# Optimization experiments

Hardware: AMD Instinct MI355X
Metric: run time of the kernel (lower is better)

## Reference

```python
import jax, jax.numpy as jnp
import numpy as np

EPS = 1e-5

def exp_map_zero(v):
    # Poincare ball exp map at origin: tanh(||v||) * v / ||v||
    norm = jnp.clip(jnp.linalg.norm(v, axis=-1, keepdims=True), EPS, None)
    return jnp.tanh(jnp.clip(norm, None, 15.0)) * v / norm

def poincare_pairwise_distance(x, c):
    # x: [N, D] points in the ball, c: [K, D] points in the ball -> [N, K]
    x2 = jnp.sum(x * x, axis=-1)                      # [N]
    c2 = jnp.sum(c * c, axis=-1)                      # [K]
    sqdiff = x2[:, None] + c2[None, :] - 2.0 * (x @ c.T)   # ||x-c||^2, [N, K]
    sqdiff = jnp.clip(sqdiff, 0.0, None)
    denom = jnp.clip((1.0 - x2)[:, None] * (1.0 - c2)[None, :], EPS, None)
    arg = jnp.clip(1.0 + 2.0 * sqdiff / denom, 1.0 + 1e-7, None)
    return jnp.arccosh(arg)

def setup_inputs() -> dict:
    key = jax.random.key(0)
    k1, k2, k3 = jax.random.split(key, 3)
    N, K, D = 200000, 128, 128
    node_repr = jax.random.normal(k1, (N, D), dtype=jnp.float32) * 0.05  # inside unit ball
    mask = jnp.ones((N, 1), dtype=jnp.float32)
    centroid_weight = jax.random.normal(k2, (K, D), dtype=jnp.float32) * 0.05
    return {"node_repr": node_repr, "mask": mask, "centroid_weight": centroid_weight}

def reference(node_repr, mask, centroid_weight):
    # euclidean embed_manifold path: map centroid params onto the ball first
    centroid_repr = exp_map_zero(centroid_weight)                  # [K, D]
    dist = poincare_pairwise_distance(node_repr, centroid_repr)    # [N, K]
    node_centroid_dist = dist[None, :, :] * mask                   # [1, N, K] (mask [N,1] broadcasts)
    graph_centroid_dist = jnp.sum(node_centroid_dist, axis=1) / jnp.sum(mask)  # [1, K]
    return (graph_centroid_dist, node_centroid_dist)
```

## Files before the change

### kernel.cpp

```cpp
#include <hip/hip_runtime.h>
#include <hip/hip_bf16.h>
#include <math.h>

#define EPSF 1e-5f

constexpr int D = 128;
constexpr int K = 128;
constexpr int ROWS_PER_BLOCK = 64;
constexpr int BPITCH = 272;

typedef __bf16 bf16x8 __attribute__((ext_vector_type(8)));
typedef float  f32x4  __attribute__((ext_vector_type(4)));

__global__ __launch_bounds__(64) void prep_kernel(const float* __restrict__ w,
                                                  __bf16* __restrict__ crb,
                                                  float* __restrict__ c2) {
    int k = blockIdx.x;
    int t = threadIdx.x;
    float a = w[k * D + t];
    float b = w[k * D + t + 64];
    float ss = a * a + b * b;
#pragma unroll
    for (int off = 1; off < 64; off <<= 1)
        ss += __shfl_xor(ss, off, 64);
    float nrm   = sqrtf(ss);
    float nclip = fmaxf(nrm, EPSF);
    float targ  = fminf(nclip, 15.0f);
    float th    = tanhf(targ);
    float s     = th / nclip;
    crb[k * D + t]      = (__bf16)(a * s);
    crb[k * D + t + 64] = (__bf16)(b * s);
    if (t == 0) {
        float cn = s * nrm;
        c2[k] = cn * cn;
    }
}

__global__ __launch_bounds__(256) void main_kernel(
        const float* __restrict__ x, const float* __restrict__ mask,
        const __bf16* __restrict__ crb, const float* __restrict__ c2g,
        float* __restrict__ out_node, float* __restrict__ partial,
        float* __restrict__ maskpart, int N) {
    __shared__ __align__(16) unsigned char sB[K * BPITCH];
    __shared__ float sX2[ROWS_PER_BLOCK];
    __shared__ float sMask[ROWS_PER_BLOCK];
    __shared__ float sC2[K];
    __shared__ float sCol[4][K];

    const int t    = threadIdx.x;
    const int wave = t >> 6;
    const int lane = t & 63;
    const int m    = lane & 15;
    const int q    = lane >> 4;
    const int nbase   = blockIdx.x * ROWS_PER_BLOCK;
    const int rowbase = nbase + wave * 16;

    const float* xrow = x + (size_t)(rowbase + m) * D + q * 8;
    float4 xr[8];
#pragma unroll
    for (int s = 0; s < 4; s++) {
        xr[2 * s]     = *(const float4*)(xrow + s * 32);
        xr[2 * s + 1] = *(const float4*)(xrow + s * 32 + 4);
    }

#pragma unroll
    for (int i = 0; i < 8; i++) {
        int f4  = t + 256 * i;
        int row = f4 >> 4;
        int c4  = f4 & 15;
        float4 v = ((const float4*)crb)[f4];
        *(float4*)(sB + row * BPITCH + c4 * 16) = v;
    }
    if (t < ROWS_PER_BLOCK) sMask[t] = mask[nbase + t];
    if (t < K) sC2[t] = c2g[t];

    float ssq = 0.f;
    bf16x8 av[4];
#pragma unroll
    for (int s = 0; s < 4; s++) {
        float4 a0 = xr[2 * s], a1 = xr[2 * s + 1];
        ssq += a0.x*a0.x + a0.y*a0.y + a0.z*a0.z + a0.w*a0.w
             + a1.x*a1.x + a1.y*a1.y + a1.z*a1.z + a1.w*a1.w;
        av[s][0] = (__bf16)a0.x; av[s][1] = (__bf16)a0.y;
        av[s][2] = (__bf16)a0.z; av[s][3] = (__bf16)a0.w;
        av[s][4] = (__bf16)a1.x; av[s][5] = (__bf16)a1.y;
        av[s][6] = (__bf16)a1.z; av[s][7] = (__bf16)a1.w;
    }
    ssq += __shfl_xor(ssq, 16, 64);
    ssq += __shfl_xor(ssq, 32, 64);
    if (lane < 16) sX2[wave * 16 + lane] = ssq;

    __syncthreads();

    f32x4 acc[8] = {};
#pragma unroll
    for (int s = 0; s < 4; s++) {
#pragma unroll
        for (int tk = 0; tk < 8; tk++) {
            bf16x8 bv = *(const bf16x8*)(sB + (tk * 16 + m) * BPITCH + q * 16 + s * 64);
            acc[tk] = __builtin_amdgcn_mfma_f32_16x16x32_bf16(av[s], bv, acc[tk], 0, 0, 0);
        }
    }

    float x2r[4], pxr[4], mvr[4];
#pragma unroll
    for (int i = 0; i < 4; i++) {
        int rl = wave * 16 + q * 4 + i;
        x2r[i] = sX2[rl];
        pxr[i] = 1.0f - x2r[i];
        mvr[i] = sMask[rl];
    }

    float dv[8][4];
    float colsum[8];
#pragma unroll
    for (int tk = 0; tk < 8; tk++) {
        int col = tk * 16 + m;
        float c2v = sC2[col];
        float pc  = 1.0f - c2v;
        colsum[tk] = 0.f;
#pragma unroll
        for (int i = 0; i < 4; i++) {
            float dot = acc[tk][i];
            float sq  = fmaxf(x2r[i] + c2v - 2.0f * dot, 0.0f);
            float den = fmaxf(pxr[i] * pc, EPSF);
            float arg = fmaf(2.0f * sq, __builtin_amdgcn_rcpf(den), 1.0f);
            arg = fmaxf(arg, 1.0f + 1e-7f);
            float dist = __logf(arg + __builtin_amdgcn_sqrtf(fmaf(arg, arg, -1.0f)));
            float val = dist * mvr[i];
            dv[tk][i] = val;
            colsum[tk] += val;
        }
    }

#pragma unroll
    for (int tk = 0; tk < 8; tk++) {
        colsum[tk] += __shfl_xor(colsum[tk], 16, 64);
        colsum[tk] += __shfl_xor(colsum[tk], 32, 64);
    }
    if (lane < 16) {
#pragma unroll
        for (int tk = 0; tk < 8; tk++)
            sCol[wave][tk * 16 + lane] = colsum[tk];
    }

    __syncthreads();

    if (t < K)
        partial[(size_t)blockIdx.x * K + t] =
            sCol[0][t] + sCol[1][t] + sCol[2][t] + sCol[3][t];
    if (t == 0) {
        float msum = 0.f;
#pragma unroll
        for (int r = 0; r < ROWS_PER_BLOCK; r++) msum += sMask[r];
        maskpart[blockIdx.x] = msum;
    }
#pragma unroll
    for (int tk = 0; tk < 8; tk++) {
        int col = tk * 16 + m;
#pragma unroll
        for (int i = 0; i < 4; i++) {
            int n = rowbase + q * 4 + i;
            __builtin_nontemporal_store(dv[tk][i], &out_node[(size_t)n * K + col]);
        }
    }
}

__global__ __launch_bounds__(256) void reduce_kernel(
        const float* __restrict__ partial, const float* __restrict__ maskpart,
        float* __restrict__ out_graph, int NB) {
    int k = blockIdx.x;
    int t = threadIdx.x;
    float s = 0.f, mm = 0.f;
    for (int b = t; b < NB; b += 256) {
        s  += partial[(size_t)b * K + k];
        mm += maskpart[b];
    }
#pragma unroll
    for (int off = 1; off < 64; off <<= 1) {
        s  += __shfl_xor(s, off, 64);
        mm += __shfl_xor(mm, off, 64);
    }
    __shared__ float rs[4], rm[4];
    int w = t >> 6;
    if ((t & 63) == 0) { rs[w] = s; rm[w] = mm; }
    __syncthreads();
    if (t == 0) {
        float st = rs[0] + rs[1] + rs[2] + rs[3];
        float mt = rm[0] + rm[1] + rm[2] + rm[3];
        out_graph[k] = st / mt;
    }
}

extern "C" void kernel_launch(void* const* d_in, const int* in_sizes, int n_in,
                              void* d_out, int out_size, void* d_ws, size_t ws_size,
                              hipStream_t stream) {
    const float* node = (const float*)d_in[0];
    const float* mask = (const float*)d_in[1];
    const float* w    = (const float*)d_in[2];
    float* out = (float*)d_out;

    int N  = in_sizes[0] / D;
    int NB = N / ROWS_PER_BLOCK;

    __bf16* crb     = (__bf16*)d_ws;
    float* c2       = (float*)(crb + K * D);
    float* partial  = c2 + K;
    float* maskpart = partial + (size_t)NB * K;

    float* out_graph = out;
    float* out_node  = out + K;

    prep_kernel<<<K, 64, 0, stream>>>(w, crb, c2);
    main_kernel<<<NB, 256, 0, stream>>>(node, mask, crb, c2, out_node,
                                        partial, maskpart, N);
    reduce_kernel<<<K, 256, 0, stream>>>(partial, maskpart, out_graph, NB);
}
```

Before: 196.8 us.

## Make main kernel persistent with software-prefetched tiles and register-resident row stats

Replaces the one-tile-per-block grid with a persistent grid of up to 1024 blocks. Each block stages the centroid matrix in LDS once, then loops over 64-row tiles, prefetching the next tile's x and mask into registers while the current tile's MFMA and epilogue run. Row norms and mask values now move through wave shuffles instead of LDS, and outputs are stored inside the epilogue. The aim is to amortize B staging, cut the per-block partial traffic and reduction size, and overlap loads with compute. The cost is more register pressure and less latency hiding from block-level parallelism.

```diff
diff --git a/kernel.cpp b/kernel.cpp
--- a/kernel.cpp
+++ b/kernel.cpp
@@ -6,8 +6,9 @@
 
 constexpr int D = 128;
 constexpr int K = 128;
-constexpr int ROWS_PER_BLOCK = 64;
+constexpr int TILE_ROWS = 64;
 constexpr int BPITCH = 272;
+constexpr int NBG = 1024;
 
 typedef __bf16 bf16x8 __attribute__((ext_vector_type(8)));
 typedef float  f32x4  __attribute__((ext_vector_type(4)));
@@ -36,32 +37,22 @@
     }
 }
 
-__global__ __launch_bounds__(256) void main_kernel(
+__global__ __launch_bounds__(256, 4) void main_kernel(
         const float* __restrict__ x, const float* __restrict__ mask,
         const __bf16* __restrict__ crb, const float* __restrict__ c2g,
         float* __restrict__ out_node, float* __restrict__ partial,
-        float* __restrict__ maskpart, int N) {
+        float* __restrict__ maskpart, int ntiles) {
     __shared__ __align__(16) unsigned char sB[K * BPITCH];
-    __shared__ float sX2[ROWS_PER_BLOCK];
-    __shared__ float sMask[ROWS_PER_BLOCK];
-    __shared__ float sC2[K];
     __shared__ float sCol[4][K];
+    __shared__ float sM[4];
 
     const int t    = threadIdx.x;
     const int wave = t >> 6;
     const int lane = t & 63;
     const int m    = lane & 15;
     const int q    = lane >> 4;
-    const int nbase   = blockIdx.x * ROWS_PER_BLOCK;
-    const int rowbase = nbase + wave * 16;
-
-    const float* xrow = x + (size_t)(rowbase + m) * D + q * 8;
-    float4 xr[8];
-#pragma unroll
-    for (int s = 0; s < 4; s++) {
-        xr[2 * s]     = *(const float4*)(xrow + s * 32);
-        xr[2 * s + 1] = *(const float4*)(xrow + s * 32 + 4);
-    }
+    const int bid  = blockIdx.x;
+    const int stride = gridDim.x;
 
 #pragma unroll
     for (int i = 0; i < 8; i++) {
@@ -71,66 +62,98 @@
         float4 v = ((const float4*)crb)[f4];
         *(float4*)(sB + row * BPITCH + c4 * 16) = v;
     }
-    if (t < ROWS_PER_BLOCK) sMask[t] = mask[nbase + t];
-    if (t < K) sC2[t] = c2g[t];
-
-    float ssq = 0.f;
+
+    float c2v[8];
+#pragma unroll
+    for (int tk = 0; tk < 8; tk++) c2v[tk] = c2g[tk * 16 + m];
+
+    float colsum[8] = {0.f, 0.f, 0.f, 0.f, 0.f, 0.f, 0.f, 0.f};
+    float msumacc = 0.f;
+
+    float4 xr[8];
+    float  mk;
     bf16x8 av[4];
-#pragma unroll
-    for (int s = 0; s < 4; s++) {
-        float4 a0 = xr[2 * s], a1 = xr[2 * s + 1];
-        ssq += a0.x*a0.x + a0.y*a0.y + a0.z*a0.z + a0.w*a0.w
-             + a1.x*a1.x + a1.y*a1.y + a1.z*a1.z + a1.w*a1.w;
-        av[s][0] = (__bf16)a0.x; av[s][1] = (__bf16)a0.y;
-        av[s][2] = (__bf16)a0.z; av[s][3] = (__bf16)a0.w;
-        av[s][4] = (__bf16)a1.x; av[s][5] = (__bf16)a1.y;
-        av[s][6] = (__bf16)a1.z; av[s][7] = (__bf16)a1.w;
-    }
-    ssq += __shfl_xor(ssq, 16, 64);
-    ssq += __shfl_xor(ssq, 32, 64);
-    if (lane < 16) sX2[wave * 16 + lane] = ssq;
+    float  x2r[4], pxr[4], mvr[4];
+
+    auto issue_loads = [&](int tl) {
+        const float* xrow = x + (size_t)(tl * TILE_ROWS + wave * 16 + m) * D + q * 8;
+#pragma unroll
+        for (int s = 0; s < 4; s++) {
+            xr[2 * s]     = *(const float4*)(xrow + s * 32);
+            xr[2 * s + 1] = *(const float4*)(xrow + s * 32 + 4);
+        }
+        mk = mask[tl * TILE_ROWS + wave * 16 + m];
+    };
+
+    auto finish_tile = [&]() {
+        float ssq = 0.f;
+#pragma unroll
+        for (int s = 0; s < 4; s++) {
+            float4 a0 = xr[2 * s], a1 = xr[2 * s + 1];
+            ssq += a0.x*a0.x + a0.y*a0.y + a0.z*a0.z + a0.w*a0.w
+                 + a1.x*a1.x + a1.y*a1.y + a1.z*a1.z + a1.w*a1.w;
+            av[s][0] = (__bf16)a0.x; av[s][1] = (__bf16)a0.y;
+            av[s][2] = (__bf16)a0.z; av[s][3] = (__bf16)a0.w;
+            av[s][4] = (__bf16)a1.x; av[s][5] = (__bf16)a1.y;
+            av[s][6] = (__bf16)a1.z; av[s][7] = (__bf16)a1.w;
+        }
+        ssq += __shfl_xor(ssq, 16, 64);
+        ssq += __shfl_xor(ssq, 32, 64);
+        float mred = mk;
+        mred += __shfl_xor(mred, 1, 64);
+        mred += __shfl_xor(mred, 2, 64);
+        mred += __shfl_xor(mred, 4, 64);
+        mred += __shfl_xor(mred, 8, 64);
+        msumacc += mred;
+#pragma unroll
+        for (int i = 0; i < 4; i++) {
+            x2r[i] = __shfl(ssq, q * 4 + i, 64);
+            pxr[i] = 1.0f - x2r[i];
+            mvr[i] = __shfl(mk, q * 4 + i, 64);
+        }
+    };
 
     __syncthreads();
 
-    f32x4 acc[8] = {};
-#pragma unroll
-    for (int s = 0; s < 4; s++) {
+    issue_loads(bid);
+    finish_tile();
+
+    for (int tile = bid; tile < ntiles; tile += stride) {
+        f32x4 acc[8] = {};
+#pragma unroll
+        for (int s = 0; s < 4; s++) {
+#pragma unroll
+            for (int tk = 0; tk < 8; tk++) {
+                bf16x8 bv = *(const bf16x8*)(sB + (tk * 16 + m) * BPITCH + q * 16 + s * 64);
+                acc[tk] = __builtin_amdgcn_mfma_f32_16x16x32_bf16(av[s], bv, acc[tk], 0, 0, 0);
+            }
+        }
+
+        int next = tile + stride;
+        bool more = next < ntiles;
+        if (more) issue_loads(next);
+
+        const int rowq = tile * TILE_ROWS + wave * 16 + q * 4;
+        float* obase = out_node + (size_t)rowq * K + m;
 #pragma unroll
         for (int tk = 0; tk < 8; tk++) {
-            bf16x8 bv = *(const bf16x8*)(sB + (tk * 16 + m) * BPITCH + q * 16 + s * 64);
-            acc[tk] = __builtin_amdgcn_mfma_f32_16x16x32_bf16(av[s], bv, acc[tk], 0, 0, 0);
-        }
-    }
-
-    float x2r[4], pxr[4], mvr[4];
-#pragma unroll
-    for (int i = 0; i < 4; i++) {
-        int rl = wave * 16 + q * 4 + i;
-        x2r[i] = sX2[rl];
-        pxr[i] = 1.0f - x2r[i];
-        mvr[i] = sMask[rl];
-    }
-
-    float dv[8][4];
-    float colsum[8];
-#pragma unroll
-    for (int tk = 0; tk < 8; tk++) {
-        int col = tk * 16 + m;
-        float c2v = sC2[col];
-        float pc  = 1.0f - c2v;
-        colsum[tk] = 0.f;
-#pragma unroll
-        for (int i = 0; i < 4; i++) {
-            float dot = acc[tk][i];
-            float sq  = fmaxf(x2r[i] + c2v - 2.0f * dot, 0.0f);
-            float den = fmaxf(pxr[i] * pc, EPSF);
-            float arg = fmaf(2.0f * sq, __builtin_amdgcn_rcpf(den), 1.0f);
-            arg = fmaxf(arg, 1.0f + 1e-7f);
-            float dist = __logf(arg + __builtin_amdgcn_sqrtf(fmaf(arg, arg, -1.0f)));
-            float val = dist * mvr[i];
-            dv[tk][i] = val;
-            colsum[tk] += val;
-        }
+            float c2c = c2v[tk];
+            float pc  = 1.0f - c2c;
+#pragma unroll
+            for (int i = 0; i < 4; i++) {
+                float dot = acc[tk][i];
+                float sq  = fmaxf(x2r[i] + c2c - 2.0f * dot, 0.0f);
+                float den = fmaxf(pxr[i] * pc, EPSF);
+                float arg = fmaf(2.0f * sq, __builtin_amdgcn_rcpf(den), 1.0f);
+                arg = fmaxf(arg, 1.0f + 1e-7f);
+                float dist = __logf(arg + __builtin_amdgcn_sqrtf(fmaf(arg, arg, -1.0f)));
+                float val = dist * mvr[i];
+                colsum[tk] += val;
+                __builtin_nontemporal_store(val, obase + (size_t)i * K + tk * 16);
+            }
+        }
+
+        if (more) finish_tile();
     }
 
 #pragma unroll
@@ -143,27 +166,15 @@
         for (int tk = 0; tk < 8; tk++)
             sCol[wave][tk * 16 + lane] = colsum[tk];
     }
+    if (lane == 0) sM[wave] = msumacc;
 
     __syncthreads();
 
     if (t < K)
-        partial[(size_t)blockIdx.x * K + t] =
+        partial[(size_t)bid * K + t] =
             sCol[0][t] + sCol[1][t] + sCol[2][t] + sCol[3][t];
-    if (t == 0) {
-        float msum = 0.f;
-#pragma unroll
-        for (int r = 0; r < ROWS_PER_BLOCK; r++) msum += sMask[r];
-        maskpart[blockIdx.x] = msum;
-    }
-#pragma unroll
-    for (int tk = 0; tk < 8; tk++) {
-        int col = tk * 16 + m;
-#pragma unroll
-        for (int i = 0; i < 4; i++) {
-            int n = rowbase + q * 4 + i;
-            __builtin_nontemporal_store(dv[tk][i], &out_node[(size_t)n * K + col]);
-        }
-    }
+    if (t == 0)
+        maskpart[bid] = sM[0] + sM[1] + sM[2] + sM[3];
 }
 
 __global__ __launch_bounds__(256) void reduce_kernel(
@@ -200,19 +211,20 @@
     const float* w    = (const float*)d_in[2];
     float* out = (float*)d_out;
 
-    int N  = in_sizes[0] / D;
-    int NB = N / ROWS_PER_BLOCK;
+    int N      = in_sizes[0] / D;
+    int ntiles = N / TILE_ROWS;
+    int nbg    = NBG < ntiles ? NBG : ntiles;
 
     __bf16* crb     = (__bf16*)d_ws;
     float* c2       = (float*)(crb + K * D);
     float* partial  = c2 + K;
-    float* maskpart = partial + (size_t)NB * K;
+    float* maskpart = partial + (size_t)nbg * K;
 
     float* out_graph = out;
     float* out_node  = out + K;
 
     prep_kernel<<<K, 64, 0, stream>>>(w, crb, c2);
-    main_kernel<<<NB, 256, 0, stream>>>(node, mask, crb, c2, out_node,
-                                        partial, maskpart, N);
-    reduce_kernel<<<K, 256, 0, stream>>>(partial, maskpart, out_graph, NB);
-}
+    main_kernel<<<nbg, 256, 0, stream>>>(node, mask, crb, c2, out_node,
+                                         partial, maskpart, ntiles);
+    reduce_kernel<<<K, 256, 0, stream>>>(partial, maskpart, out_graph, nbg);
+}
```

New measurement: 304.7 us. +54.9%, slower.
